# Optimization experiments

Hardware: AMD Instinct MI355X
Metric: run time of the kernel (lower is better)

Reference implementation:

```python
import jax, jax.numpy as jnp
import numpy as np

B, N, F_IN, F_OUT = 8, 8192, 64, 64
LN_EPS = 1e-5


def setup_inputs() -> dict:
    key = jax.random.key(0)
    k_x, k_adj, k_ws, k_wn = jax.random.split(key, 4)
    scale = 1.0 / np.sqrt(F_IN)
    return {
        "x": jax.random.normal(k_x, (B, N, F_IN), dtype=jnp.float32),
        "adj_matrix": jax.random.randint(k_adj, (N, N), 0, 2, dtype=jnp.int32),
        "W_self": jax.random.normal(k_ws, (F_IN, F_OUT), dtype=jnp.float32) * scale,
        "b_self": jnp.zeros((F_OUT,), dtype=jnp.float32),
        "W_neigh": jax.random.normal(k_wn, (F_IN, F_OUT), dtype=jnp.float32) * scale,
        "b_neigh": jnp.zeros((F_OUT,), dtype=jnp.float32),
        "ln_gamma": jnp.ones((F_OUT,), dtype=jnp.float32),
        "ln_beta": jnp.zeros((F_OUT,), dtype=jnp.float32),
    }


def reference(x, adj_matrix, W_self, b_self, W_neigh, b_neigh, ln_gamma, ln_beta):
    # GraphSAGE 'mean' conv (vectorized form of the per-node python loop):
    # agg[b,i,:] = mean over neighbors j (adj[i,j] > 0) of x[b,j,:]
    A = (adj_matrix > 0).astype(x.dtype)                 # [N, N]
    deg = A.sum(axis=1)                                  # [N]
    agg = jnp.einsum('ij,bjf->bif', A, x)                # [B, N, F_in]
    agg = agg / jnp.maximum(deg, 1.0)[None, :, None]
    neigh_out = agg @ W_neigh + b_neigh                  # [B, N, F_out]
    # nodes with no neighbors keep zeros (loop never writes them)
    neigh_out = jnp.where((deg > 0)[None, :, None], neigh_out, 0.0)
    self_out = x @ W_self + b_self                       # [B, N, F_out]
    out = jax.nn.relu(self_out + neigh_out)              # SAGE internal relu
    # GCNBlock: relu (idempotent here) -> LayerNorm; dropout is eval-mode identity
    out = jax.nn.relu(out)
    mu = out.mean(axis=-1, keepdims=True)
    var = jnp.mean((out - mu) ** 2, axis=-1, keepdims=True)
    out = (out - mu) * jax.lax.rsqrt(var + LN_EPS) * ln_gamma + ln_beta
    return out
```

## Files before the change

### kernel.cpp

```cpp
#include <hip/hip_runtime.h>

#define NN 8192

typedef __bf16 bf16x8 __attribute__((ext_vector_type(8)));
typedef float f32x4 __attribute__((ext_vector_type(4)));
typedef unsigned short u16x8 __attribute__((ext_vector_type(8)));
typedef int i32x4 __attribute__((ext_vector_type(4)));
typedef int i32x16 __attribute__((ext_vector_type(16)));

#define GLOBAL_AS __attribute__((address_space(1)))
#define LDS_AS __attribute__((address_space(3)))

__device__ __forceinline__ unsigned short f2bf(float f) {
  unsigned int u = __builtin_bit_cast(unsigned int, f);
  u += 0x7FFFu + ((u >> 16) & 1u);
  return (unsigned short)(u >> 16);
}
__device__ __forceinline__ float bf2f(unsigned short b) {
  unsigned int u = ((unsigned int)b) << 16;
  return __builtin_bit_cast(float, u);
}

__device__ __forceinline__ unsigned long long merge16(uint4 B) {
  unsigned int t0 = (B.x | (B.x >> 4)) & 0x00FF00FFu; t0 = (t0 | (t0 >> 8)) & 0xFFFFu;
  unsigned int t1 = (B.y | (B.y >> 4)) & 0x00FF00FFu; t1 = (t1 | (t1 >> 8)) & 0xFFFFu;
  unsigned int t2 = (B.z | (B.z >> 4)) & 0x00FF00FFu; t2 = (t2 | (t2 >> 8)) & 0xFFFFu;
  unsigned int t3 = (B.w | (B.w >> 4)) & 0x00FF00FFu; t3 = (t3 | (t3 >> 8)) & 0xFFFFu;
  return (unsigned long long)(t0 | (t1 << 16))
       | ((unsigned long long)(t2 | (t3 << 16)) << 32);
}

__device__ __forceinline__ i32x4 expA(unsigned int h) {
  i32x4 a;
  a[0] = (int)((((h      ) & 0xFu) * 0x204081u) & 0x01010101u);
  a[1] = (int)((((h >> 4 ) & 0xFu) * 0x204081u) & 0x01010101u);
  a[2] = (int)((((h >> 8 ) & 0xFu) * 0x204081u) & 0x01010101u);
  a[3] = (int)((((h >> 12) & 0xFu) * 0x204081u) & 0x01010101u);
  return a;
}

__global__ __launch_bounds__(256) void packprep_kernel(
    const int* __restrict__ adj, unsigned long long* __restrict__ maskT,
    float* __restrict__ degp,
    const float* __restrict__ x, const float* __restrict__ Wself,
    const float* __restrict__ bself, const float* __restrict__ Wneigh,
    char* __restrict__ Yq, unsigned short* __restrict__ Sout) {
  __shared__ __align__(16) unsigned char xb[4][2048];
  __shared__ __align__(16) unsigned short xa[64 * 64];
  __shared__ __align__(16) unsigned short bm[128 * 64];

  const unsigned int bid = blockIdx.x;
  if (bid >= 2048 || (bid & 1) == 0) {
    const int lane = threadIdx.x & 63;
    const int wv = threadIdx.x >> 6;
    const int pbk = (bid < 2048) ? (int)(bid >> 1) : (int)(bid - 1024);
    const int row0 = (pbk >> 3) << 5;
    const int c0 = (pbk & 7) << 10;
    const int Pb = (pbk & 7) << 3;
    const int* src = adj + (size_t)(row0 + (wv << 3)) * NN + c0;
#pragma unroll
    for (int r = 0; r < 8; ++r) {
#pragma unroll
      for (int c = 0; c < 4; ++c) {
        int4 v = *(const int4*)(src + (size_t)r * NN + c * 256 + lane * 4);
        unsigned int nib = (unsigned int)(v.x > 0)
                         | ((unsigned int)(v.y > 0) << 1)
                         | ((unsigned int)(v.z > 0) << 2)
                         | ((unsigned int)(v.w > 0) << 3);
        xb[wv][r * 256 + c * 64 + lane] = (unsigned char)nib;
      }
    }
    const int r = lane >> 3, k = lane & 7;
    uint4 B0 = *(const uint4*)&xb[wv][r * 256 + k * 32];
    uint4 B1 = *(const uint4*)&xb[wv][r * 256 + k * 32 + 16];
    unsigned long long w0 = merge16(B0);
    unsigned long long w1 = merge16(B1);
    const int grow = row0 + (wv << 3) + r;
    ulonglong2 e; e.x = w0; e.y = w1;
    *(ulonglong2*)&maskT[((size_t)(Pb + k) * NN + grow) * 2] = e;
    int dg = (int)__popcll(w0) + (int)__popcll(w1);
    dg += __shfl_xor(dg, 1);
    dg += __shfl_xor(dg, 2);
    dg += __shfl_xor(dg, 4);
    if (k == 0) degp[(pbk & 7) * NN + grow] = (float)dg;
    return;
  }

  const int t = threadIdx.x;
  const int pb = (int)(bid >> 1);
  const int b = pb >> 7;
  const int j0 = (pb & 127) << 6;

  {
    const float* Wsel = (t < 128) ? Wneigh : Wself;
    const int tt = t & 127;
    const int k = tt >> 1;
    const int c0 = (tt & 1) << 5;
    const int nbase = (t < 128) ? 0 : 64;
    const float4* src = (const float4*)(Wsel + k * 64 + c0);
#pragma unroll
    for (int q = 0; q < 8; ++q) {
      float4 v = src[q];
      int n0 = nbase + c0 + q * 4;
      int n;
      n = n0 + 0; bm[n * 64 + (k ^ ((n & 7) << 3))] = f2bf(v.x);
      n = n0 + 1; bm[n * 64 + (k ^ ((n & 7) << 3))] = f2bf(v.y);
      n = n0 + 2; bm[n * 64 + (k ^ ((n & 7) << 3))] = f2bf(v.z);
      n = n0 + 3; bm[n * 64 + (k ^ ((n & 7) << 3))] = f2bf(v.w);
    }
  }
  {
    const int j = t >> 2, q = t & 3;
    const float* xrow = x + ((size_t)b * NN + j0 + j) * 64 + q * 16;
    float4 v0 = *(const float4*)(xrow + 0);
    float4 v1 = *(const float4*)(xrow + 4);
    float4 v2 = *(const float4*)(xrow + 8);
    float4 v3 = *(const float4*)(xrow + 12);
    u16x8 p0, p1;
    p0[0] = f2bf(v0.x); p0[1] = f2bf(v0.y); p0[2] = f2bf(v0.z); p0[3] = f2bf(v0.w);
    p0[4] = f2bf(v1.x); p0[5] = f2bf(v1.y); p0[6] = f2bf(v1.z); p0[7] = f2bf(v1.w);
    p1[0] = f2bf(v2.x); p1[1] = f2bf(v2.y); p1[2] = f2bf(v2.z); p1[3] = f2bf(v2.w);
    p1[4] = f2bf(v3.x); p1[5] = f2bf(v3.y); p1[6] = f2bf(v3.z); p1[7] = f2bf(v3.w);
    const int base = q * 16;
    const int sw = (j & 7) << 3;
    *(u16x8*)&xa[j * 64 + (base ^ sw)] = p0;
    *(u16x8*)&xa[j * 64 + ((base + 8) ^ sw)] = p1;
  }
  __syncthreads();

  const int lane = t & 63, w = t >> 6;
  const int rl = lane & 15, hi = lane >> 4;
  f32x4 acc[8];
#pragma unroll
  for (int i = 0; i < 8; ++i) acc[i] = (f32x4){0.f, 0.f, 0.f, 0.f};

#pragma unroll
  for (int ks = 0; ks < 2; ++ks) {
    const int r = w * 16 + rl;
    const int kel = ks * 32 + hi * 8;
    bf16x8 af = __builtin_bit_cast(bf16x8, *(u16x8*)&xa[r * 64 + (kel ^ ((r & 7) << 3))]);
#pragma unroll
    for (int nf = 0; nf < 8; ++nf) {
      const int n = nf * 16 + rl;
      bf16x8 bv = __builtin_bit_cast(bf16x8, *(u16x8*)&bm[n * 64 + (kel ^ ((n & 7) << 3))]);
      acc[nf] = __builtin_amdgcn_mfma_f32_16x16x32_bf16(af, bv, acc[nf], 0, 0, 0);
    }
  }
#pragma unroll
  for (int nf = 0; nf < 8; ++nf) {
    if (nf < 4) {
      const int n = nf * 16 + rl;
      unsigned int pkt = 0;
#pragma unroll
      for (int r = 0; r < 4; ++r) {
        float v = fminf(fmaxf(acc[nf][r] * 16.0f, -127.0f), 127.0f);
        int iv = __float2int_rn(v);
        pkt |= ((unsigned int)(iv & 0xFF)) << (r * 8);
      }
      *(unsigned int*)(Yq + (size_t)(b * 64 + n) * NN + j0 + w * 16 + hi * 4) = pkt;
    } else {
      const int fo = (nf - 4) * 16 + rl;
      const float bsv = bself[fo];
#pragma unroll
      for (int r = 0; r < 4; ++r) {
        const int jj = w * 16 + hi * 4 + r;
        Sout[((size_t)b * NN + j0 + jj) * 64 + fo] = f2bf(acc[nf][r] + bsv);
      }
    }
  }
}

__global__ __launch_bounds__(256, 2) void gemm_kernel(
    const i32x4* __restrict__ mask,
    const char* __restrict__ Yq,
    unsigned short* __restrict__ Cp) {
  __shared__ __align__(16) char yL[8][8192];
  const int tid = threadIdx.x;
  const int lane = tid & 63, w = tid >> 6;
  const int nid = ((blockIdx.x & 7) << 6) + (blockIdx.x >> 3);
  const int ksp = nid >> 8;
  const int nb = (nid >> 5) & 7;
  const int mb = nid & 31;
  const int i0 = mb << 8;
  const int kbase = ksp << 12;
  const int ncol0 = nb << 6;
  const int l31 = lane & 31, l5 = lane >> 5;
  const int hs16 = l5 << 4;

  const int cst = (w << 4) + (lane >> 3);
  const char* ysrc = Yq + (size_t)(ncol0 + cst) * NN + kbase
                     + (((lane & 7) ^ (cst & 7)) << 4);
  const i32x4* mqT = mask + ((size_t)(ksp << 5)) * NN + i0 + (w << 6) + l31;

  int boff[2][4];
#pragma unroll
  for (int nf = 0; nf < 2; ++nf)
#pragma unroll
    for (int s = 0; s < 4; ++s) {
      const int col = (nf << 5) + l31;
      const int g = (s << 1) + l5;
      boff[nf][s] = (col << 7) + ((g ^ (col & 7)) << 4);
    }

  i32x16 acc[2][2];
#pragma unroll
  for (int mf = 0; mf < 2; ++mf)
#pragma unroll
    for (int nf = 0; nf < 2; ++nf)
#pragma unroll
      for (int e = 0; e < 16; ++e) acc[mf][nf][e] = 0;

#define BARRIER  __builtin_amdgcn_s_barrier()
#define MEMBAR   asm volatile("" ::: "memory")
#define WAIT_VM6 asm volatile("s_waitcnt vmcnt(6)" ::: "memory")

#define STAGE(t)                                                              \
  {                                                                           \
    __builtin_amdgcn_global_load_lds(                                         \
        (GLOBAL_AS void*)const_cast<char*>(ysrc + (size_t)((t) & 31) * 128),  \
        (LDS_AS void*)&yL[(t) & 7][w << 11], 16, 0, 0);                       \
    __builtin_amdgcn_global_load_lds(                                         \
        (GLOBAL_AS void*)const_cast<char*>(ysrc + (size_t)8 * NN              \
                                           + (size_t)((t) & 31) * 128),       \
        (LDS_AS void*)&yL[(t) & 7][(w << 11) + 1024], 16, 0, 0);              \
  }

#define LOADM(M0, M1, t)                                                      \
  { M0 = mqT[(size_t)((t) & 31) * NN]; M1 = mqT[(size_t)((t) & 31) * NN + 32]; }

#define COMPUTE(t, M0, M1)                                                    \
  {                                                                           \
    const char* yb_ = &yL[(t) & 7][0];                                        \
    __builtin_amdgcn_s_setprio(1);                                            \
    _Pragma("unroll")                                                         \
    for (int s_ = 0; s_ < 4; ++s_) {                                          \
      i32x4 b0_ = *(const i32x4*)(yb_ + boff[0][s_]);                         \
      i32x4 b1_ = *(const i32x4*)(yb_ + boff[1][s_]);                         \
      unsigned int h0_ = (unsigned int)(M0)[s_] >> hs16;                      \
      unsigned int h1_ = (unsigned int)(M1)[s_] >> hs16;                      \
      i32x4 a0_ = expA(h0_);                                                  \
      i32x4 a1_ = expA(h1_);                                                  \
      acc[0][0] = __builtin_amdgcn_mfma_i32_32x32x32_i8(a0_, b0_, acc[0][0], 0, 0, 0); \
      acc[0][1] = __builtin_amdgcn_mfma_i32_32x32x32_i8(a0_, b1_, acc[0][1], 0, 0, 0); \
      acc[1][0] = __builtin_amdgcn_mfma_i32_32x32x32_i8(a1_, b0_, acc[1][0], 0, 0, 0); \
      acc[1][1] = __builtin_amdgcn_mfma_i32_32x32x32_i8(a1_, b1_, acc[1][1], 0, 0, 0); \
    }                                                                         \
    __builtin_amdgcn_s_setprio(0);                                            \
  }

  i32x4 Ma0, Ma1, Mb0, Mb1;
  STAGE(0);
  STAGE(1);
  STAGE(2);
  LOADM(Ma0, Ma1, 0);

  for (int t2 = 0; t2 < 32; t2 += 2) {
    LOADM(Mb0, Mb1, t2 + 1);
    STAGE(t2 + 3);
    WAIT_VM6;
    BARRIER; MEMBAR;
    COMPUTE(t2, Ma0, Ma1);
    LOADM(Ma0, Ma1, t2 + 2);
    STAGE(t2 + 4);
    WAIT_VM6;
    BARRIER; MEMBAR;
    COMPUTE(t2 + 1, Mb0, Mb1);
  }
  asm volatile("s_waitcnt vmcnt(0)" ::: "memory");

#pragma unroll
  for (int mf = 0; mf < 2; ++mf)
#pragma unroll
    for (int nf = 0; nf < 2; ++nf) {
      const int col = ncol0 + (nf << 5) + l31;
#pragma unroll
      for (int r = 0; r < 16; ++r) {
        const int row = i0 + (w << 6) + (mf << 5) + (r & 3) + ((r >> 2) << 3) + (l5 << 2);
        Cp[((size_t)ksp * NN + row) * 512 + col] = f2bf((float)acc[mf][nf][r] * 0.0625f);
      }
    }
#undef BARRIER
#undef MEMBAR
#undef WAIT_VM6
#undef STAGE
#undef LOADM
#undef COMPUTE
}

__global__ __launch_bounds__(256) void epi_kernel(
    const unsigned short* __restrict__ Cp, const float* __restrict__ degp,
    const unsigned short* __restrict__ Sbf, const float* __restrict__ bneigh,
    const float* __restrict__ gamma, const float* __restrict__ beta,
    float* __restrict__ out) {
  const int lane = threadIdx.x & 63;
  const int wid = (blockIdx.x << 2) + (threadIdx.x >> 6);
  const int b = wid >> 13;
  const int i = wid & (NN - 1);
  float deg = 0.0f;
#pragma unroll
  for (int cb = 0; cb < 8; ++cb) deg += degp[cb * NN + i];
  const float rdeg = 1.0f / fmaxf(deg, 1.0f);
  const size_t cidx = (size_t)i * 512 + b * 64 + lane;
  const float c = bf2f(Cp[cidx]) + bf2f(Cp[(size_t)NN * 512 + cidx]);
  const float sv = bf2f(Sbf[((size_t)b * NN + i) * 64 + lane]);
  float v = sv + ((deg > 0.5f) ? (c * rdeg + bneigh[lane]) : 0.0f);
  v = fmaxf(v, 0.0f);
  float s1 = v, s2 = v * v;
#pragma unroll
  for (int m = 1; m < 64; m <<= 1) {
    s1 += __shfl_xor(s1, m);
    s2 += __shfl_xor(s2, m);
  }
  const float mu = s1 * 0.015625f;
  const float var = s2 * 0.015625f - mu * mu;
  const float o = (v - mu) * rsqrtf(var + 1e-5f) * gamma[lane] + beta[lane];
  out[((size_t)b * NN + i) * 64 + lane] = o;
}

extern "C" void kernel_launch(void* const* d_in, const int* in_sizes, int n_in,
                              void* d_out, int out_size, void* d_ws, size_t ws_size,
                              hipStream_t stream) {
  (void)in_sizes; (void)n_in; (void)out_size; (void)ws_size;
  const float* x      = (const float*)d_in[0];
  const int*   adj    = (const int*)d_in[1];
  const float* Wself  = (const float*)d_in[2];
  const float* bself  = (const float*)d_in[3];
  const float* Wneigh = (const float*)d_in[4];
  const float* bneigh = (const float*)d_in[5];
  const float* gamma  = (const float*)d_in[6];
  const float* beta   = (const float*)d_in[7];
  char* ws = (char*)d_ws;
  char*               Yq    = ws;
  unsigned long long* maskT = (unsigned long long*)(ws + 4194304);
  unsigned short*     Sbf   = (unsigned short*)(ws + 12582912);
  unsigned short*     Cp    = (unsigned short*)(ws + 20971520);
  float*              degp  = (float*)(ws + 37748736);
  float*              out   = (float*)d_out;

  packprep_kernel<<<dim3(3072), dim3(256), 0, stream>>>(
      adj, maskT, degp, x, Wself, bself, Wneigh, Yq, Sbf);
  gemm_kernel<<<dim3(512), dim3(256), 0, stream>>>((const i32x4*)maskT, Yq, Cp);
  epi_kernel<<<dim3(16384), dim3(256), 0, stream>>>(Cp, degp, Sbf, bneigh, gamma, beta, out);
}
```

Measured before the change: 113.2 us.

## Pack adjacency mask with wave ballots and permute Yq columns to match

The adjacency packing now has each wave scan one full row, building 64-bit masks with __ballot instead of an LDS nibble-merge pass. It computes the full-row degree directly, so the epilogue reads a single degree value instead of summing eight partials. Ballot bits are lane-interleaved, so the quantized Yq columns are permuted to match. They are staged through LDS and written with 16-byte vector stores. This removes LDS traffic and shuffle reductions in the pack stage but adds extra barriers and more scattered narrow mask stores.

```diff
diff --git a/kernel.cpp b/kernel.cpp
--- a/kernel.cpp
+++ b/kernel.cpp
@@ -5,6 +5,7 @@
 typedef __bf16 bf16x8 __attribute__((ext_vector_type(8)));
 typedef float f32x4 __attribute__((ext_vector_type(4)));
 typedef unsigned short u16x8 __attribute__((ext_vector_type(8)));
+typedef unsigned char u8x16 __attribute__((ext_vector_type(16)));
 typedef int i32x4 __attribute__((ext_vector_type(4)));
 typedef int i32x16 __attribute__((ext_vector_type(16)));
 
@@ -19,15 +20,6 @@
 __device__ __forceinline__ float bf2f(unsigned short b) {
   unsigned int u = ((unsigned int)b) << 16;
   return __builtin_bit_cast(float, u);
-}
-
-__device__ __forceinline__ unsigned long long merge16(uint4 B) {
-  unsigned int t0 = (B.x | (B.x >> 4)) & 0x00FF00FFu; t0 = (t0 | (t0 >> 8)) & 0xFFFFu;
-  unsigned int t1 = (B.y | (B.y >> 4)) & 0x00FF00FFu; t1 = (t1 | (t1 >> 8)) & 0xFFFFu;
-  unsigned int t2 = (B.z | (B.z >> 4)) & 0x00FF00FFu; t2 = (t2 | (t2 >> 8)) & 0xFFFFu;
-  unsigned int t3 = (B.w | (B.w >> 4)) & 0x00FF00FFu; t3 = (t3 | (t3 >> 8)) & 0xFFFFu;
-  return (unsigned long long)(t0 | (t1 << 16))
-       | ((unsigned long long)(t2 | (t3 << 16)) << 32);
 }
 
 __device__ __forceinline__ i32x4 expA(unsigned int h) {
@@ -45,7 +37,6 @@
     const float* __restrict__ x, const float* __restrict__ Wself,
     const float* __restrict__ bself, const float* __restrict__ Wneigh,
     char* __restrict__ Yq, unsigned short* __restrict__ Sout) {
-  __shared__ __align__(16) unsigned char xb[4][2048];
   __shared__ __align__(16) unsigned short xa[64 * 64];
   __shared__ __align__(16) unsigned short bm[128 * 64];
 
@@ -54,35 +45,27 @@
     const int lane = threadIdx.x & 63;
     const int wv = threadIdx.x >> 6;
     const int pbk = (bid < 2048) ? (int)(bid >> 1) : (int)(bid - 1024);
-    const int row0 = (pbk >> 3) << 5;
-    const int c0 = (pbk & 7) << 10;
-    const int Pb = (pbk & 7) << 3;
-    const int* src = adj + (size_t)(row0 + (wv << 3)) * NN + c0;
-#pragma unroll
-    for (int r = 0; r < 8; ++r) {
-#pragma unroll
-      for (int c = 0; c < 4; ++c) {
-        int4 v = *(const int4*)(src + (size_t)r * NN + c * 256 + lane * 4);
-        unsigned int nib = (unsigned int)(v.x > 0)
-                         | ((unsigned int)(v.y > 0) << 1)
-                         | ((unsigned int)(v.z > 0) << 2)
-                         | ((unsigned int)(v.w > 0) << 3);
-        xb[wv][r * 256 + c * 64 + lane] = (unsigned char)nib;
+    const int row = ((pbk & 7) << 10) + ((pbk >> 3) << 2) + wv;
+    const int* src = adj + (size_t)row * NN + lane * 4;
+    unsigned long long* mrow = maskT + (size_t)row * 2;
+    int dg = 0;
+#pragma unroll 4
+    for (int c = 0; c < 32; ++c) {
+      int4 v = *(const int4*)(src + c * 256);
+      unsigned long long b0 = __ballot(v.x > 0);
+      unsigned long long b1 = __ballot(v.y > 0);
+      unsigned long long b2 = __ballot(v.z > 0);
+      unsigned long long b3 = __ballot(v.w > 0);
+      dg += (int)__popcll(b0) + (int)__popcll(b1)
+          + (int)__popcll(b2) + (int)__popcll(b3);
+      if (lane < 2) {
+        ulonglong2 e;
+        e.x = lane ? b2 : b0;
+        e.y = lane ? b3 : b1;
+        *(ulonglong2*)&mrow[(size_t)(2 * c + lane) * (NN * 2)] = e;
       }
     }
-    const int r = lane >> 3, k = lane & 7;
-    uint4 B0 = *(const uint4*)&xb[wv][r * 256 + k * 32];
-    uint4 B1 = *(const uint4*)&xb[wv][r * 256 + k * 32 + 16];
-    unsigned long long w0 = merge16(B0);
-    unsigned long long w1 = merge16(B1);
-    const int grow = row0 + (wv << 3) + r;
-    ulonglong2 e; e.x = w0; e.y = w1;
-    *(ulonglong2*)&maskT[((size_t)(Pb + k) * NN + grow) * 2] = e;
-    int dg = (int)__popcll(w0) + (int)__popcll(w1);
-    dg += __shfl_xor(dg, 1);
-    dg += __shfl_xor(dg, 2);
-    dg += __shfl_xor(dg, 4);
-    if (k == 0) degp[(pbk & 7) * NN + grow] = (float)dg;
+    if (lane == 0) degp[row] = (float)dg;
     return;
   }
 
@@ -146,27 +129,45 @@
       acc[nf] = __builtin_amdgcn_mfma_f32_16x16x32_bf16(af, bv, acc[nf], 0, 0, 0);
     }
   }
-#pragma unroll
-  for (int nf = 0; nf < 8; ++nf) {
-    if (nf < 4) {
-      const int n = nf * 16 + rl;
-      unsigned int pkt = 0;
-#pragma unroll
-      for (int r = 0; r < 4; ++r) {
-        float v = fminf(fmaxf(acc[nf][r] * 16.0f, -127.0f), 127.0f);
-        int iv = __float2int_rn(v);
-        pkt |= ((unsigned int)(iv & 0xFF)) << (r * 8);
-      }
-      *(unsigned int*)(Yq + (size_t)(b * 64 + n) * NN + j0 + w * 16 + hi * 4) = pkt;
-    } else {
-      const int fo = (nf - 4) * 16 + rl;
-      const float bsv = bself[fo];
-#pragma unroll
-      for (int r = 0; r < 4; ++r) {
-        const int jj = w * 16 + hi * 4 + r;
-        Sout[((size_t)b * NN + j0 + jj) * 64 + fo] = f2bf(acc[nf][r] + bsv);
-      }
-    }
+
+  unsigned int pkts[4];
+#pragma unroll
+  for (int nf = 0; nf < 4; ++nf) {
+    unsigned int pkt = 0;
+#pragma unroll
+    for (int r = 0; r < 4; ++r) {
+      float v = fminf(fmaxf(acc[nf][r] * 16.0f, -127.0f), 127.0f);
+      int iv = __float2int_rn(v);
+      pkt |= ((unsigned int)(iv & 0xFF)) << (r * 8);
+    }
+    pkts[nf] = pkt;
+  }
+#pragma unroll
+  for (int nf = 4; nf < 8; ++nf) {
+    const int fo = (nf - 4) * 16 + rl;
+    const float bsv = bself[fo];
+#pragma unroll
+    for (int r = 0; r < 4; ++r) {
+      const int jj = w * 16 + hi * 4 + r;
+      Sout[((size_t)b * NN + j0 + jj) * 64 + fo] = f2bf(acc[nf][r] + bsv);
+    }
+  }
+
+  __syncthreads();
+  unsigned char* yq = (unsigned char*)xa;
+#pragma unroll
+  for (int nf = 0; nf < 4; ++nf) {
+    const int n = nf * 16 + rl;
+    *(unsigned int*)&yq[n * 64 + w * 16 + hi * 4] = pkts[nf];
+  }
+  __syncthreads();
+  {
+    const int n2 = t & 63, r2 = t >> 6;
+    u8x16 ov;
+#pragma unroll
+    for (int u = 0; u < 16; ++u) ov[u] = yq[n2 * 64 + r2 + 4 * u];
+    const int base = (j0 & ~255) + ((j0 & 255) >> 2);
+    *(u8x16*)(Yq + (size_t)(b * 64 + n2) * NN + base + r2 * 64) = ov;
   }
 }
 
@@ -296,9 +297,7 @@
   const int wid = (blockIdx.x << 2) + (threadIdx.x >> 6);
   const int b = wid >> 13;
   const int i = wid & (NN - 1);
-  float deg = 0.0f;
-#pragma unroll
-  for (int cb = 0; cb < 8; ++cb) deg += degp[cb * NN + i];
+  const float deg = degp[i];
   const float rdeg = 1.0f / fmaxf(deg, 1.0f);
   const size_t cidx = (size_t)i * 512 + b * 64 + lane;
   const float c = bf2f(Cp[cidx]) + bf2f(Cp[(size_t)NN * 512 + cidx]);
```

Measured after the change: 128.9 us. 1.14x slower.
